# Kernel tuning notes

Measured on AMD Instinct MI355X. Metric: run time of the kernel, lower is better.

The kernel has to match this reference:

```python
import jax, jax.numpy as jnp
import numpy as np

NUM_HEADS = 16
KEY_DIM = 64
D_MODEL = 1024  # input feature dim


def setup_inputs() -> dict:
    key = jax.random.key(0)
    ks = jax.random.split(key, 10)
    B, T = 2, 2048
    s = 0.02
    return {
        "query": jax.random.normal(ks[0], (B, T, D_MODEL), jnp.float32),
        "Wq": jax.random.normal(ks[1], (D_MODEL, NUM_HEADS * KEY_DIM), jnp.float32) * s,
        "bq": jnp.zeros((NUM_HEADS * KEY_DIM,), jnp.float32),
        "Wk": jax.random.normal(ks[2], (D_MODEL, KEY_DIM), jnp.float32) * s,
        "bk": jnp.zeros((KEY_DIM,), jnp.float32),
        "Wv": jax.random.normal(ks[3], (D_MODEL, KEY_DIM), jnp.float32) * s,
        "bv": jnp.zeros((KEY_DIM,), jnp.float32),
        "Wo": jax.random.normal(ks[4], (NUM_HEADS * KEY_DIM, NUM_HEADS * KEY_DIM), jnp.float32) * s,
        "bo": jnp.zeros((NUM_HEADS * KEY_DIM,), jnp.float32),
    }


def reference(query, Wq, bq, Wk, bk, Wv, bv, Wo, bo):
    B, Tq, _ = query.shape
    # self-attention: key = value = query
    q = query @ Wq + bq                      # [B,Tq,H*D]
    k = query @ Wk + bk                      # [B,Tk,D] (single shared head)
    v = query @ Wv + bv                      # [B,Tk,D]
    q = q.reshape(B, Tq, NUM_HEADS, KEY_DIM)
    # scores: [B,H,Tq,Tk] — K broadcast across heads (MQA)
    scores = jnp.einsum("bqhd,bkd->bhqk", q, k) / jnp.sqrt(
        jnp.asarray(KEY_DIM, jnp.float32))
    attn = jax.nn.softmax(scores, axis=-1)
    out = jnp.einsum("bhqk,bkd->bqhd", attn, v)  # [B,Tq,H,D]
    out = out.reshape(B, Tq, NUM_HEADS * KEY_DIM)
    return out @ Wo + bo
```

## Files before the change

### kernel.cpp

```cpp
#include <hip/hip_runtime.h>
#include <math.h>

#define T_SEQ 2048
#define DM 1024
#define NH 16
#define KD 64
#define MTOT 4096

typedef __attribute__((ext_vector_type(16))) float f32x16;
typedef __attribute__((ext_vector_type(8))) __bf16 bf16x8;
typedef __attribute__((ext_vector_type(2))) __bf16 bf16x2;
typedef __attribute__((ext_vector_type(2))) int i32x2;

#define MFMA32 __builtin_amdgcn_mfma_f32_32x32x16_bf16

#define QSCALE 0.1803368801111f

struct bf2 { __bf16 h, l; };
__device__ __forceinline__ bf2 split2(float v) {
  bf2 r;
  r.h = (__bf16)v;
  r.l = (__bf16)(v - (float)r.h);
  return r;
}

__device__ __forceinline__ unsigned pkbf(__bf16 a, __bf16 b) {
  bf16x2 t;
  t[0] = a;
  t[1] = b;
  return __builtin_bit_cast(unsigned, t);
}

__device__ __forceinline__ float fexp2(float x) {
#if __has_builtin(__builtin_amdgcn_exp2f)
  return __builtin_amdgcn_exp2f(x);
#else
  return __expf(0.69314718056f * x);
#endif
}

__device__ __forceinline__ void plswap(unsigned& a, unsigned& b) {
  i32x2 r = __builtin_amdgcn_permlane32_swap((int)a, (int)b, false, false);
  a = (unsigned)r[0];
  b = (unsigned)r[1];
}

__device__ __forceinline__ f32x16 zero16() {
  f32x16 z;
#pragma unroll
  for (int i = 0; i < 16; ++i) z[i] = 0.f;
  return z;
}

__device__ __forceinline__ int drow(int reg, int l5) {
  return (reg & 3) + 8 * (reg >> 2) + 4 * l5;
}

__device__ __forceinline__ void gload16(const void* g, void* l) {
  __builtin_amdgcn_global_load_lds(
      (const __attribute__((address_space(1))) unsigned int*)g,
      (__attribute__((address_space(3))) unsigned int*)l, 16, 0, 0);
}

__device__ __forceinline__ int swzc(int row, int c) {
  return (((((c >> 3) ^ row) & 7)) << 3) | (c & 7);
}

__device__ __forceinline__ float ldf(const void* p, size_t i, int fl) {
  return fl ? ((const float*)p)[i] : (float)(((const __bf16*)p)[i]);
}

__global__ void detect_prep(const unsigned short* __restrict__ w, int* flag,
                            const void* bq, const void* bk, const void* bv,
                            const void* bo, float* bqf, float* bkf,
                            float* bvf, float* bof) {
  __shared__ int s;
  if (threadIdx.x == 0) s = 0;
  __syncthreads();
  int bad = 0;
  for (int i = threadIdx.x; i < 4096; i += 256) {
    unsigned e = (w[i] >> 7) & 0xFF;
    if (e >= 0xC0) bad = 1;
  }
  if (bad) atomicOr(&s, 1);
  __syncthreads();
  const int fl = s;
  if (threadIdx.x == 0) *flag = fl;
  for (int i = threadIdx.x; i < 1024; i += 256) {
    bqf[i] = ldf(bq, i, fl);
    bof[i] = ldf(bo, i, fl);
  }
  if (threadIdx.x < 64) {
    bkf[threadIdx.x] = ldf(bk, threadIdx.x, fl);
    bvf[threadIdx.x] = ldf(bv, threadIdx.x, fl);
  }
}

__global__ __launch_bounds__(256) void asplit_u(
    const int* __restrict__ flag, const void* __restrict__ A,
    __bf16* __restrict__ Ah) {
  const int fl = *flag;
  const int gid = blockIdx.x * 256 + threadIdx.x;
  const int row = gid >> 7;
  const int c0 = (gid & 127) * 8;
  bf16x8 h;
  if (fl) {
    const float* Af = (const float*)A + (size_t)row * 1024 + c0;
    float4 v0 = *reinterpret_cast<const float4*>(Af);
    float4 v1 = *reinterpret_cast<const float4*>(Af + 4);
    h[0] = (__bf16)v0.x; h[1] = (__bf16)v0.y;
    h[2] = (__bf16)v0.z; h[3] = (__bf16)v0.w;
    h[4] = (__bf16)v1.x; h[5] = (__bf16)v1.y;
    h[6] = (__bf16)v1.z; h[7] = (__bf16)v1.w;
  } else {
    h = *reinterpret_cast<const bf16x8*>((const __bf16*)A + (size_t)row * 1024 + c0);
  }
  const int cb = (c0 & ~63) | (swzc(row & 7, c0 & 63) & ~7);
  *reinterpret_cast<bf16x8*>(Ah + (size_t)row * 1024 + cb) = h;
}

__global__ __launch_bounds__(256) void tsplit_u(
    const int* __restrict__ flag, const void* __restrict__ Wq,
    const void* __restrict__ Wk, const void* __restrict__ Wv,
    const void* __restrict__ Wo, __bf16* __restrict__ wqkv,
    __bf16* __restrict__ woh, __bf16* __restrict__ wol) {
  __shared__ float ts[32][33];
  const int fl = *flag;
  const int t = threadIdx.x;
  const int y = blockIdx.y;
  const void* W;
  int N, n0, rowoff;
  bool lo = false;
  __bf16* dh;
  if (y < 32)      { W = Wq; N = 1024; n0 = y * 32;        rowoff = 0;    dh = wqkv; }
  else if (y < 34) { W = Wk; N = 64;   n0 = (y - 32) * 32; rowoff = 1024; dh = wqkv; }
  else if (y < 36) { W = Wv; N = 64;   n0 = (y - 34) * 32; rowoff = 1088; dh = wqkv; }
  else             { W = Wo; N = 1024; n0 = (y - 36) * 32; rowoff = 0;    dh = woh; lo = true; }
  const int k0 = blockIdx.x * 32;
#pragma unroll
  for (int i = 0; i < 4; ++i) {
    int idx = t + 256 * i;
    int r = idx >> 5, c = idx & 31;
    ts[r][c] = ldf(W, (size_t)(k0 + r) * N + n0 + c, fl);
  }
  __syncthreads();
#pragma unroll
  for (int i = 0; i < 4; ++i) {
    int idx = t + 256 * i;
    int r = idx >> 5, c = idx & 31;
    bf2 s = split2(ts[c][r]);
    const int rr = rowoff + n0 + r, cc = k0 + c;
    const int sc = (cc & ~63) | swzc(rr & 7, cc & 63);
    dh[(size_t)rr * 1024 + sc] = s.h;
    if (lo) wol[(size_t)rr * 1024 + sc] = s.l;
  }
}

__global__ __launch_bounds__(256, 4) void gemmqkv(
    const __bf16* __restrict__ Ah_g, const __bf16* __restrict__ Bh_g,
    const float* __restrict__ bqf, const float* __restrict__ bkf,
    const float* __restrict__ bvf,
    __bf16* __restrict__ Qh, __bf16* __restrict__ Kh2,
    __bf16* __restrict__ Vh2) {
  __shared__ __bf16 As[128][64], Bs[64][64];
  const int t = threadIdx.x, l = t & 63, w = t >> 6;
  const int l31 = l & 31, l5 = l >> 5, l7 = l31 & 7;
  const int m0 = blockIdx.x * 128, n0 = blockIdx.y * 64;

  f32x16 acc[2];
  acc[0] = zero16();
  acc[1] = zero16();

  for (int k0 = 0; k0 < 1024; k0 += 64) {
    __syncthreads();
    const int c8 = (t & 7) * 8;
#pragma unroll
    for (int i = 0; i < 4; ++i) {
      const int idx = i * 256 + t;
      gload16(Ah_g + (size_t)(m0 + (idx >> 3)) * 1024 + k0 + c8, (__bf16*)As + idx * 8);
    }
#pragma unroll
    for (int i = 0; i < 2; ++i) {
      const int idx = i * 256 + t;
      gload16(Bh_g + (size_t)(n0 + (idx >> 3)) * 1024 + k0 + c8, (__bf16*)Bs + idx * 8);
    }
    __syncthreads();
#pragma unroll
    for (int kb = 0; kb < 4; ++kb) {
      const int p = ((2 * kb + l5) ^ l7) * 8;
      bf16x8 ah = *reinterpret_cast<const bf16x8*>(&As[w * 32 + l31][p]);
#pragma unroll
      for (int nt = 0; nt < 2; ++nt) {
        bf16x8 bh = *reinterpret_cast<const bf16x8*>(&Bs[nt * 32 + l31][p]);
        acc[nt] = MFMA32(ah, bh, acc[nt], 0, 0, 0);
      }
    }
  }
#pragma unroll
  for (int nt = 0; nt < 2; ++nt) {
    const int cbase = n0 + nt * 32;
    const int col = cbase + l31;
    if (cbase < 1024) {
      const float bb = bqf[col];
#pragma unroll
      for (int reg = 0; reg < 16; ++reg) {
        const int mrow = m0 + w * 32 + drow(reg, l5);
        Qh[(size_t)mrow * 1024 + col] = (__bf16)((acc[nt][reg] + bb) * QSCALE);
      }
    } else if (cbase < 1088) {
      const int d = col - 1024;
      const float bb = bkf[d];
#pragma unroll
      for (int reg = 0; reg < 16; ++reg) {
        const int mrow = m0 + w * 32 + drow(reg, l5);
        Kh2[(size_t)mrow * 64 + swzc(mrow & 7, d)] = (__bf16)(acc[nt][reg] + bb);
      }
    } else {
      const int d = col - 1088;
      const float bb = bvf[d];
#pragma unroll
      for (int reg = 0; reg < 16; ++reg) {
        const int mrow = m0 + w * 32 + drow(reg, l5);
        const int bb2 = mrow >> 11, tt = mrow & 2047;
        const int sct = (tt & ~63) | swzc(d & 7, tt & 63);
        Vh2[((size_t)bb2 * 64 + d) * 2048 + sct] = (__bf16)(acc[nt][reg] + bb);
      }
    }
  }
}

__global__ __launch_bounds__(256, 2) void gemmwo(
    const int* __restrict__ flag,
    const __bf16* __restrict__ Ahi, const __bf16* __restrict__ Alo,
    const __bf16* __restrict__ Bh, const __bf16* __restrict__ Bl,
    const float* __restrict__ bof, void* __restrict__ CT) {
  __shared__ __bf16 Ah[128][64], Al[128][64];
  __shared__ __bf16 Bth[64][64], Btl[64][64];
  const int t = threadIdx.x, l = t & 63, w = t >> 6;
  const int l31 = l & 31, l5 = l >> 5, l7 = l31 & 7;
  const int m0 = blockIdx.x * 128, n0 = blockIdx.y * 64;

  f32x16 acc[2];
  acc[0] = zero16();
  acc[1] = zero16();

  for (int k0 = 0; k0 < 1024; k0 += 64) {
    __syncthreads();
    const int c8 = (t & 7) * 8;
#pragma unroll
    for (int i = 0; i < 4; ++i) {
      const int idx = i * 256 + t;
      const size_t ga = (size_t)(m0 + (idx >> 3)) * 1024 + k0 + c8;
      gload16(Ahi + ga, (__bf16*)Ah + idx * 8);
      gload16(Alo + ga, (__bf16*)Al + idx * 8);
    }
#pragma unroll
    for (int i = 0; i < 2; ++i) {
      const int idx = i * 256 + t;
      const size_t gb = (size_t)(n0 + (idx >> 3)) * 1024 + k0 + c8;
      gload16(Bh + gb, (__bf16*)Bth + idx * 8);
      gload16(Bl + gb, (__bf16*)Btl + idx * 8);
    }
    __syncthreads();
#pragma unroll
    for (int kb = 0; kb < 4; ++kb) {
      const int p = ((2 * kb + l5) ^ l7) * 8;
      bf16x8 ah = *reinterpret_cast<const bf16x8*>(&Ah[w * 32 + l31][p]);
      bf16x8 al = *reinterpret_cast<const bf16x8*>(&Al[w * 32 + l31][p]);
#pragma unroll
      for (int nt = 0; nt < 2; ++nt) {
        bf16x8 bh = *reinterpret_cast<const bf16x8*>(&Bth[nt * 32 + l31][p]);
        bf16x8 bl = *reinterpret_cast<const bf16x8*>(&Btl[nt * 32 + l31][p]);
        acc[nt] = MFMA32(al, bh, acc[nt], 0, 0, 0);
        acc[nt] = MFMA32(ah, bl, acc[nt], 0, 0, 0);
        acc[nt] = MFMA32(ah, bh, acc[nt], 0, 0, 0);
      }
    }
  }
  const int fl = *flag;
#pragma unroll
  for (int nt = 0; nt < 2; ++nt) {
    const int col = n0 + nt * 32 + l31;
    const float bb = bof[col];
#pragma unroll
    for (int reg = 0; reg < 16; ++reg) {
      const int mrow = m0 + w * 32 + drow(reg, l5);
      const float v = acc[nt][reg] + bb;
      if (fl) ((float*)CT)[(size_t)mrow * 1024 + col] = v;
      else ((__bf16*)CT)[(size_t)mrow * 1024 + col] = (__bf16)v;
    }
  }
}

__global__ __launch_bounds__(512, 2) void attn8(
    const __bf16* __restrict__ Qh_g, const __bf16* __restrict__ Kh_g,
    const __bf16* __restrict__ Vh_g,
    __bf16* __restrict__ AOhi, __bf16* __restrict__ AOlo) {
  __shared__ alignas(16) char arena[98304];
  const int t = threadIdx.x, l = t & 63, w = t >> 6;
  const int wq = w & 3, kvh = w >> 2;
  const int l31 = l & 31, l5 = l >> 5, l7 = l31 & 7;
  const int tl = t & 255;
  const int q0 = blockIdx.x * 256;
  const int h = blockIdx.y, b = blockIdx.z;

  __bf16* Kbase = (__bf16*)(arena + kvh * 16384);
  __bf16* Vbase = (__bf16*)(arena + 32768 + kvh * 16384);

  bf16x8 onesb;
#pragma unroll
  for (int j = 0; j < 8; ++j) onesb[j] = (__bf16)1.0f;

  bf16x8 qh0[4], qh1[4];
  {
    const size_t qa = ((size_t)(b * T_SEQ + q0 + wq * 64 + l31)) * DM + h * KD;
#pragma unroll
    for (int ks = 0; ks < 4; ++ks) {
      qh0[ks] = *reinterpret_cast<const bf16x8*>(Qh_g + qa + ks * 16 + l5 * 8);
      qh1[ks] = *reinterpret_cast<const bf16x8*>(Qh_g + qa + (size_t)32 * DM + ks * 16 + l5 * 8);
    }
  }

  f32x16 o0 = zero16(), o1 = zero16(), o2 = zero16(), o3 = zero16();
  f32x16 lacca = zero16(), laccb = zero16();

  const __bf16* Kg = Kh_g + (size_t)b * T_SEQ * KD;
  const __bf16* Vg = Vh_g + (size_t)b * KD * T_SEQ;
  const int sc8 = (tl & 7) * 8;
  const int kbase = kvh * 1024;

#define ASTAGE(BUF, KT0)                                                       \
  {                                                                            \
    const int r0 = tl >> 3, r1 = (256 + tl) >> 3;                              \
    gload16(Kg + (size_t)((KT0) + r0) * KD + sc8, Kbase + (BUF)*4096 + tl * 8);\
    gload16(Kg + (size_t)((KT0) + r1) * KD + sc8,                              \
            Kbase + (BUF)*4096 + (256 + tl) * 8);                              \
    gload16(Vg + (size_t)r0 * T_SEQ + (KT0) + sc8, Vbase + (BUF)*4096 + tl * 8);\
    gload16(Vg + (size_t)r1 * T_SEQ + (KT0) + sc8,                             \
            Vbase + (BUF)*4096 + (256 + tl) * 8);                              \
  }

  ASTAGE(0, kbase);
  __syncthreads();
  int cur = 0;

  for (int kt = 0; kt < 1024; kt += 64) {
    if (kt + 64 < 1024) ASTAGE(cur ^ 1, kbase + kt + 64);

#pragma unroll
    for (int hf = 0; hf < 2; ++hf) {
      f32x16 sva = zero16(), svb = zero16();
      __builtin_amdgcn_s_setprio(1);
#pragma unroll
      for (int ks = 0; ks < 4; ++ks) {
        const int p = ((2 * ks + l5) ^ l7) * 8;
        bf16x8 kh = *reinterpret_cast<const bf16x8*>(
            Kbase + cur * 4096 + (hf * 32 + l31) * 64 + p);
        sva = MFMA32(kh, qh0[ks], sva, 0, 0, 0);
        svb = MFMA32(kh, qh1[ks], svb, 0, 0, 0);
      }
      __builtin_amdgcn_s_setprio(0);
      unsigned uha[8], uhb[8];
#pragma unroll
      for (int g2 = 0; g2 < 8; ++g2) {
        float a0 = fexp2(fminf(sva[2 * g2], 43.f));
        float a1 = fexp2(fminf(sva[2 * g2 + 1], 43.f));
        uha[g2] = pkbf((__bf16)a0, (__bf16)a1);
        float b0 = fexp2(fminf(svb[2 * g2], 43.f));
        float b1 = fexp2(fminf(svb[2 * g2 + 1], 43.f));
        uhb[g2] = pkbf((__bf16)b0, (__bf16)b1);
      }
#pragma unroll
      for (int kc = 0; kc < 2; ++kc) {
        unsigned a0 = uha[4 * kc], a1 = uha[4 * kc + 1];
        unsigned a2 = uha[4 * kc + 2], a3 = uha[4 * kc + 3];
        plswap(a0, a2);
        plswap(a1, a3);
        alignas(16) unsigned fa[4] = {a0, a1, a2, a3};
        bf16x8 pa = *reinterpret_cast<bf16x8*>(fa);
        unsigned b0 = uhb[4 * kc], b1 = uhb[4 * kc + 1];
        unsigned b2 = uhb[4 * kc + 2], b3 = uhb[4 * kc + 3];
        plswap(b0, b2);
        plswap(b1, b3);
        alignas(16) unsigned fb[4] = {b0, b1, b2, b3};
        bf16x8 pb = *reinterpret_cast<bf16x8*>(fb);

        const int kk = 2 * hf + kc;
        const int p = ((2 * kk + l5) ^ l7) * 8;
        bf16x8 v0 = *reinterpret_cast<const bf16x8*>(Vbase + cur * 4096 + l31 * 64 + p);
        bf16x8 v1 = *reinterpret_cast<const bf16x8*>(Vbase + cur * 4096 + (32 + l31) * 64 + p);
        __builtin_amdgcn_s_setprio(1);
        lacca = MFMA32(pa, onesb, lacca, 0, 0, 0);
        o0 = MFMA32(pa, v0, o0, 0, 0, 0);
        o1 = MFMA32(pa, v1, o1, 0, 0, 0);
        laccb = MFMA32(pb, onesb, laccb, 0, 0, 0);
        o2 = MFMA32(pb, v0, o2, 0, 0, 0);
        o3 = MFMA32(pb, v1, o3, 0, 0, 0);
        __builtin_amdgcn_s_setprio(0);
      }
    }
    __syncthreads();
    cur ^= 1;
  }

  float* ex = (float*)arena;
  float* exl = (float*)(arena + 65536);
  if (kvh == 1) {
#pragma unroll
    for (int g = 0; g < 4; ++g) {
      int cc0 = (0 + g + l) & 15;
      *reinterpret_cast<float4*>(&ex[((wq * 64 + l) << 6) + cc0 * 4]) =
          make_float4(o0[4 * g], o0[4 * g + 1], o0[4 * g + 2], o0[4 * g + 3]);
      int cc1 = (4 + g + l) & 15;
      *reinterpret_cast<float4*>(&ex[((wq * 64 + l) << 6) + cc1 * 4]) =
          make_float4(o1[4 * g], o1[4 * g + 1], o1[4 * g + 2], o1[4 * g + 3]);
      int cc2 = (8 + g + l) & 15;
      *reinterpret_cast<float4*>(&ex[((wq * 64 + l) << 6) + cc2 * 4]) =
          make_float4(o2[4 * g], o2[4 * g + 1], o2[4 * g + 2], o2[4 * g + 3]);
      int cc3 = (12 + g + l) & 15;
      *reinterpret_cast<float4*>(&ex[((wq * 64 + l) << 6) + cc3 * 4]) =
          make_float4(o3[4 * g], o3[4 * g + 1], o3[4 * g + 2], o3[4 * g + 3]);
      int s0 = (g + l) & 7;
      *reinterpret_cast<float4*>(&exl[((wq * 64 + l) << 5) + s0 * 4]) =
          make_float4(lacca[4 * g], lacca[4 * g + 1], lacca[4 * g + 2], lacca[4 * g + 3]);
      int s1 = (4 + g + l) & 7;
      *reinterpret_cast<float4*>(&exl[((wq * 64 + l) << 5) + s1 * 4]) =
          make_float4(laccb[4 * g], laccb[4 * g + 1], laccb[4 * g + 2], laccb[4 * g + 3]);
    }
  }
  __syncthreads();
  if (kvh == 0) {
#pragma unroll
    for (int g = 0; g < 4; ++g) {
      int cc0 = (0 + g + l) & 15;
      float4 v = *reinterpret_cast<float4*>(&ex[((wq * 64 + l) << 6) + cc0 * 4]);
      o0[4 * g] += v.x; o0[4 * g + 1] += v.y; o0[4 * g + 2] += v.z; o0[4 * g + 3] += v.w;
      int cc1 = (4 + g + l) & 15;
      v = *reinterpret_cast<float4*>(&ex[((wq * 64 + l) << 6) + cc1 * 4]);
      o1[4 * g] += v.x; o1[4 * g + 1] += v.y; o1[4 * g + 2] += v.z; o1[4 * g + 3] += v.w;
      int cc2 = (8 + g + l) & 15;
      v = *reinterpret_cast<float4*>(&ex[((wq * 64 + l) << 6) + cc2 * 4]);
      o2[4 * g] += v.x; o2[4 * g + 1] += v.y; o2[4 * g + 2] += v.z; o2[4 * g + 3] += v.w;
      int cc3 = (12 + g + l) & 15;
      v = *reinterpret_cast<float4*>(&ex[((wq * 64 + l) << 6) + cc3 * 4]);
      o3[4 * g] += v.x; o3[4 * g + 1] += v.y; o3[4 * g + 2] += v.z; o3[4 * g + 3] += v.w;
      int s0 = (g + l) & 7;
      v = *reinterpret_cast<float4*>(&exl[((wq * 64 + l) << 5) + s0 * 4]);
      lacca[4 * g] += v.x; lacca[4 * g + 1] += v.y;
      lacca[4 * g + 2] += v.z; lacca[4 * g + 3] += v.w;
      int s1 = (4 + g + l) & 7;
      v = *reinterpret_cast<float4*>(&exl[((wq * 64 + l) << 5) + s1 * 4]);
      laccb[4 * g] += v.x; laccb[4 * g + 1] += v.y;
      laccb[4 * g + 2] += v.z; laccb[4 * g + 3] += v.w;
    }
#pragma unroll
    for (int reg = 0; reg < 16; ++reg) {
      const int rq = drow(reg, l5);
      const int cl = ((((l31 >> 3) ^ rq) & 7) << 3) | (l31 & 7);
      const int ch = ((((4 + (l31 >> 3)) ^ rq) & 7) << 3) | (l31 & 7);
      const float inva = 1.f / lacca[reg];
      const size_t roa = ((size_t)(b * T_SEQ + q0 + wq * 64 + rq)) * DM + h * KD;
      bf2 s;
      s = split2(o0[reg] * inva); AOhi[roa + cl] = s.h; AOlo[roa + cl] = s.l;
      s = split2(o1[reg] * inva); AOhi[roa + ch] = s.h; AOlo[roa + ch] = s.l;
      const float invb = 1.f / laccb[reg];
      const size_t rob = roa + (size_t)32 * DM;
      s = split2(o2[reg] * invb); AOhi[rob + cl] = s.h; AOlo[rob + cl] = s.l;
      s = split2(o3[reg] * invb); AOhi[rob + ch] = s.h; AOlo[rob + ch] = s.l;
    }
  }
#undef ASTAGE
}

extern "C" void kernel_launch(void* const* d_in, const int* in_sizes, int n_in,
                              void* d_out, int out_size, void* d_ws, size_t ws_size,
                              hipStream_t stream) {
  char* ws = (char*)d_ws;
  int* flag = (int*)ws;
  size_t o = 4096;
  float* bqf = (float*)(ws + o); o += 4096;
  float* bkf = (float*)(ws + o); o += 4096;
  float* bvf = (float*)(ws + o); o += 4096;
  float* bof = (float*)(ws + o); o += 4096;
  __bf16* wqkvt_h = (__bf16*)(ws + o); o += (size_t)1152 * 1024 * 2;
  __bf16* wot_h = (__bf16*)(ws + o); o += 2097152;
  __bf16* wot_l = (__bf16*)(ws + o); o += 2097152;
  __bf16* khi = (__bf16*)(ws + o); o += 524288;
  __bf16* vthi = (__bf16*)(ws + o); o += 524288;
  __bf16* ahi = (__bf16*)(ws + o); o += 8388608;
  __bf16* aolo = (__bf16*)(ws + o); o += 8388608;
  __bf16* qhi = (__bf16*)(ws + o); o += 8388608;
  __bf16* aohi = ahi;

  detect_prep<<<1, 256, 0, stream>>>(
      (const unsigned short*)d_in[1], flag, d_in[2], d_in[4], d_in[6], d_in[8],
      bqf, bkf, bvf, bof);
  asplit_u<<<2048, 256, 0, stream>>>(flag, d_in[0], ahi);
  tsplit_u<<<dim3(32, 68), 256, 0, stream>>>(
      flag, d_in[1], d_in[3], d_in[5], d_in[7], wqkvt_h, wot_h, wot_l);
  gemmqkv<<<dim3(32, 18), 256, 0, stream>>>(
      ahi, wqkvt_h, bqf, bkf, bvf, qhi, khi, vthi);
  attn8<<<dim3(T_SEQ / 256, NH, 2), 512, 0, stream>>>(
      qhi, khi, vthi, aohi, aolo);
  gemmwo<<<dim3(32, 16), 256, 0, stream>>>(
      flag, aohi, aolo, wot_h, wot_l, bof, d_out);
}
```

Measured before the change: 198.0 us.

## Merge prep kernels, shrink attention LDS arena, raise gemmwo occupancy

Merges the activation-cast kernel and the weight-transpose kernel into a single launch by giving the activation work extra grid rows, which removes one kernel launch. The attention kernel's cross-half softmax-denominator exchange now stores a single per-row value instead of replicated per-lane data. That lets the LDS arena shrink from 96KB to 65KB, with the aim of fitting more blocks per CU. gemmwo's launch bounds are raised to 3 blocks per SM, which may force register spills.

Measured after the change: 191.1 us. 1.04x faster.

```diff
diff --git a/kernel.cpp b/kernel.cpp
--- a/kernel.cpp
+++ b/kernel.cpp
@@ -96,38 +96,36 @@
   }
 }
 
-__global__ __launch_bounds__(256) void asplit_u(
-    const int* __restrict__ flag, const void* __restrict__ A,
-    __bf16* __restrict__ Ah) {
-  const int fl = *flag;
-  const int gid = blockIdx.x * 256 + threadIdx.x;
-  const int row = gid >> 7;
-  const int c0 = (gid & 127) * 8;
-  bf16x8 h;
-  if (fl) {
-    const float* Af = (const float*)A + (size_t)row * 1024 + c0;
-    float4 v0 = *reinterpret_cast<const float4*>(Af);
-    float4 v1 = *reinterpret_cast<const float4*>(Af + 4);
-    h[0] = (__bf16)v0.x; h[1] = (__bf16)v0.y;
-    h[2] = (__bf16)v0.z; h[3] = (__bf16)v0.w;
-    h[4] = (__bf16)v1.x; h[5] = (__bf16)v1.y;
-    h[6] = (__bf16)v1.z; h[7] = (__bf16)v1.w;
-  } else {
-    h = *reinterpret_cast<const bf16x8*>((const __bf16*)A + (size_t)row * 1024 + c0);
-  }
-  const int cb = (c0 & ~63) | (swzc(row & 7, c0 & 63) & ~7);
-  *reinterpret_cast<bf16x8*>(Ah + (size_t)row * 1024 + cb) = h;
-}
-
-__global__ __launch_bounds__(256) void tsplit_u(
-    const int* __restrict__ flag, const void* __restrict__ Wq,
-    const void* __restrict__ Wk, const void* __restrict__ Wv,
-    const void* __restrict__ Wo, __bf16* __restrict__ wqkv,
+__global__ __launch_bounds__(256) void prep_u(
+    const int* __restrict__ flag, const void* __restrict__ Aq,
+    const void* __restrict__ Wq, const void* __restrict__ Wk,
+    const void* __restrict__ Wv, const void* __restrict__ Wo,
+    __bf16* __restrict__ Ah, __bf16* __restrict__ wqkv,
     __bf16* __restrict__ woh, __bf16* __restrict__ wol) {
-  __shared__ float ts[32][33];
   const int fl = *flag;
   const int t = threadIdx.x;
   const int y = blockIdx.y;
+  if (y >= 68) {
+    const int gid = ((y - 68) * 32 + blockIdx.x) * 256 + t;
+    const int row = gid >> 7;
+    const int c0 = (gid & 127) * 8;
+    bf16x8 h;
+    if (fl) {
+      const float* Af = (const float*)Aq + (size_t)row * 1024 + c0;
+      float4 v0 = *reinterpret_cast<const float4*>(Af);
+      float4 v1 = *reinterpret_cast<const float4*>(Af + 4);
+      h[0] = (__bf16)v0.x; h[1] = (__bf16)v0.y;
+      h[2] = (__bf16)v0.z; h[3] = (__bf16)v0.w;
+      h[4] = (__bf16)v1.x; h[5] = (__bf16)v1.y;
+      h[6] = (__bf16)v1.z; h[7] = (__bf16)v1.w;
+    } else {
+      h = *reinterpret_cast<const bf16x8*>((const __bf16*)Aq + (size_t)row * 1024 + c0);
+    }
+    const int cb = (c0 & ~63) | (swzc(row & 7, c0 & 63) & ~7);
+    *reinterpret_cast<bf16x8*>(Ah + (size_t)row * 1024 + cb) = h;
+    return;
+  }
+  __shared__ float ts[32][33];
   const void* W;
   int N, n0, rowoff;
   bool lo = false;
@@ -229,7 +227,7 @@
   }
 }
 
-__global__ __launch_bounds__(256, 2) void gemmwo(
+__global__ __launch_bounds__(256, 3) void gemmwo(
     const int* __restrict__ flag,
     const __bf16* __restrict__ Ahi, const __bf16* __restrict__ Alo,
     const __bf16* __restrict__ Bh, const __bf16* __restrict__ Bl,
@@ -296,7 +294,7 @@
     const __bf16* __restrict__ Qh_g, const __bf16* __restrict__ Kh_g,
     const __bf16* __restrict__ Vh_g,
     __bf16* __restrict__ AOhi, __bf16* __restrict__ AOlo) {
-  __shared__ alignas(16) char arena[98304];
+  __shared__ alignas(16) char arena[66560];
   const int t = threadIdx.x, l = t & 63, w = t >> 6;
   const int wq = w & 3, kvh = w >> 2;
   const int l31 = l & 31, l5 = l >> 5, l7 = l31 & 7;
@@ -420,12 +418,13 @@
       int cc3 = (12 + g + l) & 15;
       *reinterpret_cast<float4*>(&ex[((wq * 64 + l) << 6) + cc3 * 4]) =
           make_float4(o3[4 * g], o3[4 * g + 1], o3[4 * g + 2], o3[4 * g + 3]);
-      int s0 = (g + l) & 7;
-      *reinterpret_cast<float4*>(&exl[((wq * 64 + l) << 5) + s0 * 4]) =
-          make_float4(lacca[4 * g], lacca[4 * g + 1], lacca[4 * g + 2], lacca[4 * g + 3]);
-      int s1 = (4 + g + l) & 7;
-      *reinterpret_cast<float4*>(&exl[((wq * 64 + l) << 5) + s1 * 4]) =
-          make_float4(laccb[4 * g], laccb[4 * g + 1], laccb[4 * g + 2], laccb[4 * g + 3]);
+    }
+    if (l31 == 0) {
+#pragma unroll
+      for (int r = 0; r < 16; ++r) {
+        exl[(wq * 2 + l5) * 32 + r] = lacca[r];
+        exl[(wq * 2 + l5) * 32 + 16 + r] = laccb[r];
+      }
     }
   }
   __syncthreads();
@@ -444,14 +443,11 @@
       int cc3 = (12 + g + l) & 15;
       v = *reinterpret_cast<float4*>(&ex[((wq * 64 + l) << 6) + cc3 * 4]);
       o3[4 * g] += v.x; o3[4 * g + 1] += v.y; o3[4 * g + 2] += v.z; o3[4 * g + 3] += v.w;
-      int s0 = (g + l) & 7;
-      v = *reinterpret_cast<float4*>(&exl[((wq * 64 + l) << 5) + s0 * 4]);
-      lacca[4 * g] += v.x; lacca[4 * g + 1] += v.y;
-      lacca[4 * g + 2] += v.z; lacca[4 * g + 3] += v.w;
-      int s1 = (4 + g + l) & 7;
-      v = *reinterpret_cast<float4*>(&exl[((wq * 64 + l) << 5) + s1 * 4]);
-      laccb[4 * g] += v.x; laccb[4 * g + 1] += v.y;
-      laccb[4 * g + 2] += v.z; laccb[4 * g + 3] += v.w;
+    }
+#pragma unroll
+    for (int r = 0; r < 16; ++r) {
+      lacca[r] += exl[(wq * 2 + l5) * 32 + r];
+      laccb[r] += exl[(wq * 2 + l5) * 32 + 16 + r];
     }
 #pragma unroll
     for (int reg = 0; reg < 16; ++reg) {
@@ -495,9 +491,9 @@
   detect_prep<<<1, 256, 0, stream>>>(
       (const unsigned short*)d_in[1], flag, d_in[2], d_in[4], d_in[6], d_in[8],
       bqf, bkf, bvf, bof);
-  asplit_u<<<2048, 256, 0, stream>>>(flag, d_in[0], ahi);
-  tsplit_u<<<dim3(32, 68), 256, 0, stream>>>(
-      flag, d_in[1], d_in[3], d_in[5], d_in[7], wqkvt_h, wot_h, wot_l);
+  prep_u<<<dim3(32, 132), 256, 0, stream>>>(
+      flag, d_in[0], d_in[1], d_in[3], d_in[5], d_in[7],
+      ahi, wqkvt_h, wot_h, wot_l);
   gemmqkv<<<dim3(32, 18), 256, 0, stream>>>(
       ahi, wqkvt_h, bqf, bkf, bvf, qhi, khi, vthi);
   attn8<<<dim3(T_SEQ / 256, NH, 2), 512, 0, stream>>>(
```
